# Performance work log

Measured on AMD Instinct MI355X. Metric: run time of the kernel, lower is better.

The kernel has to match this reference:

```python
import jax, jax.numpy as jnp
import numpy as np

N_EMBD = 768
N_HEAD = 12
HEAD_DIM = N_EMBD // N_HEAD  # 64


def apply_rotary_emb(x, cos, sin):
    d = x.shape[-1] // 2
    x1, x2 = x[..., :d], x[..., d:]
    y1 = x1 * cos + x2 * sin
    y2 = x1 * -sin + x2 * cos
    return jnp.concatenate([y1, y2], axis=-1)


def rms_norm(x):
    return x * jax.lax.rsqrt(jnp.mean(jnp.square(x), axis=-1, keepdims=True) + 1e-06)


def setup_inputs() -> dict:
    key = jax.random.key(0)
    ks = jax.random.split(key, 7)
    B, T = 2, 2048
    x = jax.random.normal(ks[0], (B, T, N_EMBD), dtype=jnp.float32)
    # cos/sin broadcast over (B, head) axes of [B, T, H, HEAD_DIM//2]
    cos = jax.random.uniform(ks[1], (T, 1, HEAD_DIM // 2), dtype=jnp.float32)
    sin = jax.random.uniform(ks[2], (T, 1, HEAD_DIM // 2), dtype=jnp.float32)
    scale = 1.0 / np.sqrt(N_EMBD)
    wq = jax.random.normal(ks[3], (N_EMBD, N_EMBD), dtype=jnp.float32) * scale
    wk = jax.random.normal(ks[4], (N_EMBD, N_EMBD), dtype=jnp.float32) * scale
    wv = jax.random.normal(ks[5], (N_EMBD, N_EMBD), dtype=jnp.float32) * scale
    wproj = jax.random.normal(ks[6], (N_EMBD, N_EMBD), dtype=jnp.float32) * scale
    return {"x": x, "cos": cos, "sin": sin, "wq": wq, "wk": wk, "wv": wv, "wproj": wproj}


def reference(x, cos, sin, wq, wk, wv, wproj):
    B, T, C = x.shape
    q = (x @ wq).reshape(B, T, N_HEAD, HEAD_DIM)
    k = (x @ wk).reshape(B, T, N_HEAD, HEAD_DIM)
    v = (x @ wv).reshape(B, T, N_HEAD, HEAD_DIM)
    q = rms_norm(apply_rotary_emb(q, cos, sin))
    k = rms_norm(apply_rotary_emb(k, cos, sin))
    # [B, H, T, T] attention scores (non-causal, as in source)
    attn = jnp.einsum('bqhd,bkhd->bhqk', q, k) / jnp.sqrt(jnp.float32(HEAD_DIM))
    attn = jax.nn.softmax(attn, axis=-1)
    y = jnp.einsum('bhqk,bkhd->bqhd', attn, v).reshape(B, T, C)
    return y @ wproj
```

## Files before the change

kernel.cpp:

```cpp
#include <hip/hip_runtime.h>
#include <hip/hip_bf16.h>
#include <stdint.h>

typedef __attribute__((ext_vector_type(8))) __bf16 bf16x8;
typedef __attribute__((ext_vector_type(4))) __bf16 bf16x4;
typedef __attribute__((ext_vector_type(2))) __bf16 bf16x2;
typedef __attribute__((ext_vector_type(4))) float f32x4;
typedef __attribute__((ext_vector_type(16))) float f32x16;
typedef __attribute__((ext_vector_type(8))) unsigned short u16x8;
typedef __attribute__((ext_vector_type(4))) unsigned int u32x4;

#define DEVI __device__ __forceinline__

DEVI void gload16(const void* g, void* l) {
  __builtin_amdgcn_global_load_lds((const __attribute__((address_space(1))) void*)g,
                                   (__attribute__((address_space(3))) void*)l, 16, 0, 0);
}

DEVI uint32_t pack2(float a, float b) {
  bf16x2 t;
  t[0] = (__bf16)a;
  t[1] = (__bf16)b;
  return __builtin_bit_cast(uint32_t, t);
}

DEVI int vswz(int d) { return ((d ^ (d >> 3)) & 15) << 4; }

__global__ __launch_bounds__(256) void prep_k(const float* __restrict__ x,
                                              const float* __restrict__ wq,
                                              const float* __restrict__ wk,
                                              const float* __restrict__ wv,
                                              const float* __restrict__ wp,
                                              __bf16* __restrict__ xb,
                                              __bf16* __restrict__ WT) {
  __shared__ float tile[32][33];
  const int bid = blockIdx.x, tid = threadIdx.x;
  if (bid < 2304) {
    const int z = bid / 576, r = bid % 576;
    const int bx = r % 24, by = r / 24;
    const float* W = (z == 0) ? wq : (z == 1) ? wk : (z == 2) ? wv : wp;
    int n0 = bx * 32, k0 = by * 32;
    int tx = tid & 31, ty = tid >> 5;
#pragma unroll
    for (int j = 0; j < 4; ++j)
      tile[ty + 8 * j][tx] = W[(size_t)(k0 + ty + 8 * j) * 768 + n0 + tx];
    __syncthreads();
#pragma unroll
    for (int j = 0; j < 4; ++j)
      WT[(size_t)(z * 768 + n0 + ty + 8 * j) * 768 + k0 + tx] =
          (__bf16)tile[tx][ty + 8 * j];
  } else {
    const int n4 = (4096 * 768) / 4;
    int i = (bid - 2304) * 256 + tid;
    for (; i < n4; i += 768 * 256) {
      float4 v = ((const float4*)x)[i];
      bf16x4 o;
      o[0] = (__bf16)v.x; o[1] = (__bf16)v.y; o[2] = (__bf16)v.z; o[3] = (__bf16)v.w;
      ((bf16x4*)xb)[i] = o;
    }
  }
}

template <int EPI, int BN>
__global__ __launch_bounds__(256) void gemm_k(const __bf16* __restrict__ A,
                                              const __bf16* __restrict__ B,
                                              void* __restrict__ Cout,
                                              const float* __restrict__ cosT,
                                              const float* __restrict__ sinT,
                                              int K, int lda, int ldb, int ldc,
                                              int nwg, int nxb) {
  constexpr int NF = BN / 32;
  constexpr int LPT = 2 + BN / 64;
  __shared__ __align__(16) __bf16 Al[4][128 * 32];
  __shared__ __align__(16) __bf16 Bl[4][BN * 32];
  const int tid = threadIdx.x, lane = tid & 63, w = tid >> 6;
  const int wm = w >> 1, wn = w & 1;
  const int bid = blockIdx.x;
  const int o = (bid & 7) * (nwg >> 3) + (bid >> 3);
  const int bx = o % nxb, by = o / nxb;
  const int m0 = by * 128, n0 = bx * BN;
  const int c = lane & 15, g = lane >> 4;
  f32x4 acc[4][NF] = {};

  auto stage = [&](int k0, int buf) {
#pragma unroll
    for (int i = 0; i < 2; ++i) {
      int e = (i * 256 + tid) * 8;
      int row = e >> 5, col = e & 31;
      gload16(A + (size_t)(m0 + row) * lda + k0 + col, (char*)&Al[buf][0] + 2 * (size_t)e);
    }
#pragma unroll
    for (int i = 0; i < BN / 64; ++i) {
      int e = (i * 256 + tid) * 8;
      int row = e >> 5, col = e & 31;
      gload16(B + (size_t)(n0 + row) * ldb + k0 + col, (char*)&Bl[buf][0] + 2 * (size_t)e);
    }
  };

  const int NIT = K / 32;
  stage(0, 0);
  stage(32, 1);
  for (int t = 0; t < NIT; ++t) {
    if (t + 2 < NIT) {
      stage((t + 2) * 32, (t + 2) & 3);
      asm volatile("s_waitcnt vmcnt(%0)" ::"i"(2 * LPT) : "memory");
    } else if (t + 1 < NIT) {
      asm volatile("s_waitcnt vmcnt(%0)" ::"i"(LPT) : "memory");
    } else {
      asm volatile("s_waitcnt vmcnt(0)" ::: "memory");
    }
    __builtin_amdgcn_s_barrier();
    const int cur = t & 3;
    bf16x8 af[4], bfr[NF];
#pragma unroll
    for (int q = 0; q < 4; ++q)
      af[q] = *(const bf16x8*)&Al[cur][(wm * 64 + q * 16 + c) * 32 + 8 * g];
#pragma unroll
    for (int q = 0; q < NF; ++q)
      bfr[q] = *(const bf16x8*)&Bl[cur][(wn * (BN / 2) + q * 16 + c) * 32 + 8 * g];
#pragma unroll
    for (int mf = 0; mf < 4; ++mf)
#pragma unroll
      for (int nf = 0; nf < NF; ++nf)
        acc[mf][nf] = __builtin_amdgcn_mfma_f32_16x16x32_bf16(af[mf], bfr[nf],
                                                              acc[mf][nf], 0, 0, 0);
  }

  if (EPI == 1) {
    __bf16* out = (__bf16*)Cout;
    const int colbase = n0 + wn * 64;
    const int plane = colbase / 768;
#pragma unroll
    for (int mf = 0; mf < 4; ++mf) {
#pragma unroll
      for (int r = 0; r < 4; ++r) {
        int row = m0 + wm * 64 + mf * 16 + 4 * g + r;
        float v0 = acc[mf][0][r], v1 = acc[mf][1][r], v2 = acc[mf][2][r], v3 = acc[mf][3][r];
        float y0, y1, y2, y3;
        if (plane < 2) {
          int t = row & 2047;
          float c0 = cosT[t * 32 + c],      s0 = sinT[t * 32 + c];
          float c1 = cosT[t * 32 + 16 + c], s1 = sinT[t * 32 + 16 + c];
          y0 = v0 * c0 + v2 * s0;
          y2 = v2 * c0 - v0 * s0;
          y1 = v1 * c1 + v3 * s1;
          y3 = v3 * c1 - v1 * s1;
          float ss = y0 * y0 + y1 * y1 + y2 * y2 + y3 * y3;
          ss += __shfl_xor(ss, 1); ss += __shfl_xor(ss, 2);
          ss += __shfl_xor(ss, 4); ss += __shfl_xor(ss, 8);
          float rn = rsqrtf(ss * (1.0f / 64.0f) + 1e-6f);
          y0 *= rn; y1 *= rn; y2 *= rn; y3 *= rn;
        } else {
          y0 = v0; y1 = v1; y2 = v2; y3 = v3;
        }
        size_t base = (size_t)row * ldc + colbase + c;
        out[base +  0] = (__bf16)y0;
        out[base + 16] = (__bf16)y1;
        out[base + 32] = (__bf16)y2;
        out[base + 48] = (__bf16)y3;
      }
    }
  } else {
    float* out = (float*)Cout;
#pragma unroll
    for (int mf = 0; mf < 4; ++mf)
#pragma unroll
      for (int nf = 0; nf < NF; ++nf)
#pragma unroll
        for (int r = 0; r < 4; ++r) {
          int row = m0 + wm * 64 + mf * 16 + 4 * g + r;
          out[(size_t)row * ldc + n0 + wn * (BN / 2) + nf * 16 + c] = acc[mf][nf][r];
        }
  }
}

__global__ __launch_bounds__(256, 2) void attn_k(const __bf16* __restrict__ QKV,
                                                 __bf16* __restrict__ Yb) {
  constexpr int TT = 2048, KVB = 128, NT = TT / KVB;
  __shared__ __align__(16) char smem[65536];
  const int tid = threadIdx.x, lane = tid & 63, w = tid >> 6;
  const int q5 = lane & 31, h = lane >> 5;
  const int bid = blockIdx.x;
  const int xcd = bid & 7, idx = bid >> 3;
  const int bh = xcd * 3 + (idx >> 4), qb = idx & 15;
  const int b = bh / 12, hd = bh % 12;
  const size_t ldq = 2304;
  const __bf16* Qg = QKV + (size_t)(b * TT) * ldq + hd * 64;
  const __bf16* Kg = QKV + (size_t)(b * TT) * ldq + 768 + hd * 64;
  const __bf16* Vg = QKV + (size_t)(b * TT) * ldq + 1536 + hd * 64;

  const int qrow = qb * 128 + w * 32 + q5;
  bf16x8 aq[4];
#pragma unroll
  for (int t = 0; t < 4; ++t)
    aq[t] = *(const bf16x8*)(Qg + (size_t)qrow * ldq + t * 16 + 8 * h);

  u16x8 vr[4];
  auto stageK = [&](int kv0, int buf) {
#pragma unroll
    for (int p = 0; p < 4; ++p) {
      int cid = p * 256 + tid;
      int row = cid >> 3, s = cid & 7;
      int srccol = 8 * (s ^ (row & 7));
      gload16(Kg + (size_t)(kv0 + row) * ldq + srccol,
              smem + buf * 16384 + row * 128 + 16 * s);
    }
  };
  auto loadV = [&](int kv0) {
#pragma unroll
    for (int p = 0; p < 2; ++p) {
      int u = p * 256 + tid;
      int kp = u >> 3, d0 = (u & 7) * 8;
      const __bf16* src0 = Vg + (size_t)(kv0 + 2 * kp) * ldq + d0;
      vr[2 * p] = *(const u16x8*)src0;
      vr[2 * p + 1] = *(const u16x8*)(src0 + ldq);
    }
  };
  auto writeV = [&](int buf) {
    char* vb = smem + 32768 + buf * 16384;
#pragma unroll
    for (int p = 0; p < 2; ++p) {
      int u = p * 256 + tid;
      int kp = u >> 3, d0 = (u & 7) * 8;
#pragma unroll
      for (int i = 0; i < 8; ++i) {
        int d = d0 + i;
        int byte = (d * 256 + 4 * kp) ^ vswz(d);
        uint32_t pk = (uint32_t)vr[2 * p][i] | ((uint32_t)vr[2 * p + 1][i] << 16);
        *(uint32_t*)(vb + byte) = pk;
      }
    }
  };

  f32x16 Yacc[2] = {};
  const float SC = 0.18033688f;
  float m2 = -__builtin_inff(), l_run = 0.f;

  stageK(0, 0);
  loadV(0);
  writeV(0);
  __syncthreads();

  f32x16 Sv[4];
#define SV(i) Sv[(i) >> 4][(i) & 15]

  for (int t = 0; t < NT; ++t) {
    const int cur = t & 1;
    const char* Kb = smem + cur * 16384;
    const char* Vb = smem + 32768 + cur * 16384;
    if (t + 1 < NT) {
      stageK((t + 1) * KVB, cur ^ 1);
      loadV((t + 1) * KVB);
    }

#pragma unroll
    for (int j = 0; j < 4; ++j) {
      f32x16 S = {};
#pragma unroll
      for (int tt = 0; tt < 4; ++tt) {
        int row = j * 32 + q5;
        int chunk = (2 * tt + h) ^ (q5 & 7);
        bf16x8 kf = *(const bf16x8*)(Kb + row * 128 + 16 * chunk);
        S = __builtin_amdgcn_mfma_f32_32x32x16_bf16(kf, aq[tt], S, 0, 0, 0);
      }
      Sv[j] = S;
    }

    float m0 = SV(0), m1 = SV(1), m2c = SV(2), m3 = SV(3);
#pragma unroll
    for (int i = 4; i < 64; i += 4) {
      m0 = fmaxf(m0, SV(i));       m1 = fmaxf(m1, SV(i + 1));
      m2c = fmaxf(m2c, SV(i + 2)); m3 = fmaxf(m3, SV(i + 3));
    }
    float mx = fmaxf(fmaxf(m0, m1), fmaxf(m2c, m3));
    mx = fmaxf(mx, __shfl_xor(mx, 32));
    mx *= SC;
    if (!__all(mx <= m2 + 8.0f)) {
      float mn = fmaxf(m2, mx);
      float corr = __builtin_exp2f(m2 - mn);
      l_run *= corr;
#pragma unroll
      for (int dh = 0; dh < 2; ++dh)
#pragma unroll
        for (int r = 0; r < 16; ++r) Yacc[dh][r] *= corr;
      m2 = mn;
    }
    float rs0 = 0.f, rs1 = 0.f, rs2 = 0.f, rs3 = 0.f;
#pragma unroll
    for (int i = 0; i < 64; i += 4) {
      float e0 = __builtin_exp2f(fmaf(SV(i), SC, -m2));
      float e1 = __builtin_exp2f(fmaf(SV(i + 1), SC, -m2));
      float e2 = __builtin_exp2f(fmaf(SV(i + 2), SC, -m2));
      float e3 = __builtin_exp2f(fmaf(SV(i + 3), SC, -m2));
      SV(i) = e0; SV(i + 1) = e1; SV(i + 2) = e2; SV(i + 3) = e3;
      rs0 += e0; rs1 += e1; rs2 += e2; rs3 += e3;
    }
    float rs = (rs0 + rs1) + (rs2 + rs3);
    rs += __shfl_xor(rs, 32);
    l_run += rs;

#pragma unroll
    for (int j = 0; j < 4; ++j) {
#pragma unroll
      for (int s = 0; s < 2; ++s) {
        int e0 = j * 16 + s * 8;
        uint32_t pk01 = pack2(SV(e0 + 0), SV(e0 + 1));
        uint32_t pk23 = pack2(SV(e0 + 2), SV(e0 + 3));
        uint32_t pk45 = pack2(SV(e0 + 4), SV(e0 + 5));
        uint32_t pk67 = pack2(SV(e0 + 6), SV(e0 + 7));
        uint32_t fa = (uint32_t)__shfl_xor((int)(h ? pk01 : pk45), 32);
        uint32_t fb = (uint32_t)__shfl_xor((int)(h ? pk23 : pk67), 32);
        u32x4 pw;
        pw[0] = h ? fa : pk01;
        pw[1] = h ? fb : pk23;
        pw[2] = h ? pk45 : fa;
        pw[3] = h ? pk67 : fb;
        bf16x8 pfrag = __builtin_bit_cast(bf16x8, pw);
        int keyb = j * 64 + s * 32 + 16 * h;
#pragma unroll
        for (int dh = 0; dh < 2; ++dh) {
          int d = dh * 32 + q5;
          int byte = (d * 256 + keyb) ^ vswz(d);
          bf16x8 vf = *(const bf16x8*)(Vb + byte);
          Yacc[dh] = __builtin_amdgcn_mfma_f32_32x32x16_bf16(vf, pfrag, Yacc[dh], 0, 0, 0);
        }
      }
    }
    if (t + 1 < NT) writeV(cur ^ 1);
    __syncthreads();
  }
#undef SV

  float rl = __builtin_amdgcn_rcpf(l_run);
  char* yb = smem + w * (32 * 144);
#pragma unroll
  for (int dh = 0; dh < 2; ++dh)
#pragma unroll
    for (int a = 0; a < 4; ++a) {
      bf16x4 pkv;
#pragma unroll
      for (int i = 0; i < 4; ++i) pkv[i] = (__bf16)(Yacc[dh][a * 4 + i] * rl);
      int d0 = a * 8 + 4 * h + 32 * dh;
      *(bf16x4*)(yb + q5 * 144 + d0 * 2) = pkv;
    }
  __bf16* Yrow = Yb + (size_t)(b * TT + qb * 128 + w * 32) * 768 + hd * 64;
#pragma unroll
  for (int k = 0; k < 4; ++k) {
    int chunk = k * 64 + lane;
    int qr = chunk >> 3, sr = chunk & 7;
    bf16x8 vv = *(const bf16x8*)(yb + qr * 144 + sr * 16);
    *(bf16x8*)(Yrow + (size_t)qr * 768 + sr * 8) = vv;
  }
}

extern "C" void kernel_launch(void* const* d_in, const int* in_sizes, int n_in,
                              void* d_out, int out_size, void* d_ws, size_t ws_size,
                              hipStream_t stream) {
  const float* x = (const float*)d_in[0];
  const float* cosT = (const float*)d_in[1];
  const float* sinT = (const float*)d_in[2];
  const float* wq = (const float*)d_in[3];
  const float* wk = (const float*)d_in[4];
  const float* wv = (const float*)d_in[5];
  const float* wp = (const float*)d_in[6];

  char* ws = (char*)d_ws;
  __bf16* xb   = (__bf16*)(ws);
  __bf16* WT   = (__bf16*)(ws + 6291456);
  __bf16* QKVb = (__bf16*)(ws + 11010048);
  __bf16* Yb   = (__bf16*)(ws + 29884416);

  prep_k<<<3072, 256, 0, stream>>>(x, wq, wk, wv, wp, xb, WT);
  gemm_k<1, 128><<<576, 256, 0, stream>>>(xb, WT, (void*)QKVb, cosT, sinT,
                                          768, 768, 768, 2304, 576, 18);
  attn_k<<<384, 256, 0, stream>>>(QKVb, Yb);
  gemm_k<0, 64><<<384, 256, 0, stream>>>(Yb, WT + (size_t)2304 * 768, d_out,
                                         nullptr, nullptr, 768, 768, 768, 768, 384, 12);
}
```

Baseline: 200.7 us.

## Write V transposed from QKV GEMM epilogue and stage it via async LDS loads

New measurement: 190.7 us. 5.0% less time.

```diff
diff --git a/kernel.cpp b/kernel.cpp
--- a/kernel.cpp
+++ b/kernel.cpp
@@ -7,7 +7,6 @@
 typedef __attribute__((ext_vector_type(2))) __bf16 bf16x2;
 typedef __attribute__((ext_vector_type(4))) float f32x4;
 typedef __attribute__((ext_vector_type(16))) float f32x16;
-typedef __attribute__((ext_vector_type(8))) unsigned short u16x8;
 typedef __attribute__((ext_vector_type(4))) unsigned int u32x4;
 
 #define DEVI __device__ __forceinline__
@@ -23,8 +22,6 @@
   t[1] = (__bf16)b;
   return __builtin_bit_cast(uint32_t, t);
 }
-
-DEVI int vswz(int d) { return ((d ^ (d >> 3)) & 15) << 4; }
 
 __global__ __launch_bounds__(256) void prep_k(const float* __restrict__ x,
                                               const float* __restrict__ wq,
@@ -65,6 +62,7 @@
 __global__ __launch_bounds__(256) void gemm_k(const __bf16* __restrict__ A,
                                               const __bf16* __restrict__ B,
                                               void* __restrict__ Cout,
+                                              __bf16* __restrict__ Vt,
                                               const float* __restrict__ cosT,
                                               const float* __restrict__ sinT,
                                               int K, int lda, int ldb, int ldc,
@@ -127,37 +125,48 @@
   }
 
   if (EPI == 1) {
-    __bf16* out = (__bf16*)Cout;
     const int colbase = n0 + wn * 64;
     const int plane = colbase / 768;
-#pragma unroll
-    for (int mf = 0; mf < 4; ++mf) {
-#pragma unroll
-      for (int r = 0; r < 4; ++r) {
-        int row = m0 + wm * 64 + mf * 16 + 4 * g + r;
-        float v0 = acc[mf][0][r], v1 = acc[mf][1][r], v2 = acc[mf][2][r], v3 = acc[mf][3][r];
-        float y0, y1, y2, y3;
-        if (plane < 2) {
+    if (plane == 2) {
+      const int hd = (colbase - 1536) >> 6;
+#pragma unroll
+      for (int mf = 0; mf < 4; ++mf)
+#pragma unroll
+        for (int nf = 0; nf < 4; ++nf) {
+          bf16x4 pk;
+#pragma unroll
+          for (int r = 0; r < 4; ++r) pk[r] = (__bf16)acc[mf][nf][r];
+          int row = m0 + wm * 64 + mf * 16 + 4 * g;
+          int bb = row >> 11, tloc = row & 2047;
+          int d = nf * 16 + c;
+          *(bf16x4*)(Vt + ((size_t)(bb * 12 + hd) * 64 + d) * 2048 + tloc) = pk;
+        }
+    } else {
+      __bf16* out = (__bf16*)Cout;
+#pragma unroll
+      for (int mf = 0; mf < 4; ++mf) {
+#pragma unroll
+        for (int r = 0; r < 4; ++r) {
+          int row = m0 + wm * 64 + mf * 16 + 4 * g + r;
+          float v0 = acc[mf][0][r], v1 = acc[mf][1][r], v2 = acc[mf][2][r], v3 = acc[mf][3][r];
           int t = row & 2047;
           float c0 = cosT[t * 32 + c],      s0 = sinT[t * 32 + c];
           float c1 = cosT[t * 32 + 16 + c], s1 = sinT[t * 32 + 16 + c];
-          y0 = v0 * c0 + v2 * s0;
-          y2 = v2 * c0 - v0 * s0;
-          y1 = v1 * c1 + v3 * s1;
-          y3 = v3 * c1 - v1 * s1;
+          float y0 = v0 * c0 + v2 * s0;
+          float y2 = v2 * c0 - v0 * s0;
+          float y1 = v1 * c1 + v3 * s1;
+          float y3 = v3 * c1 - v1 * s1;
           float ss = y0 * y0 + y1 * y1 + y2 * y2 + y3 * y3;
           ss += __shfl_xor(ss, 1); ss += __shfl_xor(ss, 2);
           ss += __shfl_xor(ss, 4); ss += __shfl_xor(ss, 8);
           float rn = rsqrtf(ss * (1.0f / 64.0f) + 1e-6f);
           y0 *= rn; y1 *= rn; y2 *= rn; y3 *= rn;
-        } else {
-          y0 = v0; y1 = v1; y2 = v2; y3 = v3;
+          size_t base = (size_t)row * ldc + colbase + c;
+          out[base +  0] = (__bf16)y0;
+          out[base + 16] = (__bf16)y1;
+          out[base + 32] = (__bf16)y2;
+          out[base + 48] = (__bf16)y3;
         }
-        size_t base = (size_t)row * ldc + colbase + c;
-        out[base +  0] = (__bf16)y0;
-        out[base + 16] = (__bf16)y1;
-        out[base + 32] = (__bf16)y2;
-        out[base + 48] = (__bf16)y3;
       }
     }
   } else {
@@ -174,20 +183,19 @@
   }
 }
 
-__global__ __launch_bounds__(256, 2) void attn_k(const __bf16* __restrict__ QKV,
+__global__ __launch_bounds__(256, 2) void attn_k(const __bf16* __restrict__ QK,
+                                                 const __bf16* __restrict__ Vt,
                                                  __bf16* __restrict__ Yb) {
   constexpr int TT = 2048, KVB = 128, NT = TT / KVB;
   __shared__ __align__(16) char smem[65536];
   const int tid = threadIdx.x, lane = tid & 63, w = tid >> 6;
   const int q5 = lane & 31, h = lane >> 5;
-  const int bid = blockIdx.x;
-  const int xcd = bid & 7, idx = bid >> 3;
-  const int bh = xcd * 3 + (idx >> 4), qb = idx & 15;
+  const int qb = blockIdx.x, bh = blockIdx.y;
   const int b = bh / 12, hd = bh % 12;
-  const size_t ldq = 2304;
-  const __bf16* Qg = QKV + (size_t)(b * TT) * ldq + hd * 64;
-  const __bf16* Kg = QKV + (size_t)(b * TT) * ldq + 768 + hd * 64;
-  const __bf16* Vg = QKV + (size_t)(b * TT) * ldq + 1536 + hd * 64;
+  const size_t ldq = 1536;
+  const __bf16* Qg = QK + (size_t)(b * TT) * ldq + hd * 64;
+  const __bf16* Kg = QK + (size_t)(b * TT) * ldq + 768 + hd * 64;
+  const __bf16* Vtg = Vt + (size_t)(b * 12 + hd) * 64 * 2048;
 
   const int qrow = qb * 128 + w * 32 + q5;
   bf16x8 aq[4];
@@ -195,40 +203,22 @@
   for (int t = 0; t < 4; ++t)
     aq[t] = *(const bf16x8*)(Qg + (size_t)qrow * ldq + t * 16 + 8 * h);
 
-  u16x8 vr[4];
   auto stageK = [&](int kv0, int buf) {
 #pragma unroll
     for (int p = 0; p < 4; ++p) {
       int cid = p * 256 + tid;
       int row = cid >> 3, s = cid & 7;
-      int srccol = 8 * (s ^ (row & 7));
-      gload16(Kg + (size_t)(kv0 + row) * ldq + srccol,
-              smem + buf * 16384 + row * 128 + 16 * s);
+      gload16(Kg + (size_t)(kv0 + row) * ldq + 8 * (s ^ (row & 7)),
+              smem + buf * 16384 + cid * 16);
     }
   };
-  auto loadV = [&](int kv0) {
-#pragma unroll
-    for (int p = 0; p < 2; ++p) {
-      int u = p * 256 + tid;
-      int kp = u >> 3, d0 = (u & 7) * 8;
-      const __bf16* src0 = Vg + (size_t)(kv0 + 2 * kp) * ldq + d0;
-      vr[2 * p] = *(const u16x8*)src0;
-      vr[2 * p + 1] = *(const u16x8*)(src0 + ldq);
-    }
-  };
-  auto writeV = [&](int buf) {
-    char* vb = smem + 32768 + buf * 16384;
-#pragma unroll
-    for (int p = 0; p < 2; ++p) {
-      int u = p * 256 + tid;
-      int kp = u >> 3, d0 = (u & 7) * 8;
-#pragma unroll
-      for (int i = 0; i < 8; ++i) {
-        int d = d0 + i;
-        int byte = (d * 256 + 4 * kp) ^ vswz(d);
-        uint32_t pk = (uint32_t)vr[2 * p][i] | ((uint32_t)vr[2 * p + 1][i] << 16);
-        *(uint32_t*)(vb + byte) = pk;
-      }
+  auto stageVt = [&](int kv0, int buf) {
+#pragma unroll
+    for (int p = 0; p < 4; ++p) {
+      int cid = p * 256 + tid;
+      int row = cid >> 4, cc = cid & 15;
+      gload16(Vtg + (size_t)row * 2048 + kv0 + 8 * (cc ^ (row & 15)),
+              smem + 32768 + buf * 16384 + cid * 16);
     }
   };
 
@@ -237,8 +227,7 @@
   float m2 = -__builtin_inff(), l_run = 0.f;
 
   stageK(0, 0);
-  loadV(0);
-  writeV(0);
+  stageVt(0, 0);
   __syncthreads();
 
   f32x16 Sv[4];
@@ -250,7 +239,7 @@
     const char* Vb = smem + 32768 + cur * 16384;
     if (t + 1 < NT) {
       stageK((t + 1) * KVB, cur ^ 1);
-      loadV((t + 1) * KVB);
+      stageVt((t + 1) * KVB, cur ^ 1);
     }
 
 #pragma unroll
@@ -316,17 +305,15 @@
         pw[2] = h ? pk45 : fa;
         pw[3] = h ? pk67 : fb;
         bf16x8 pfrag = __builtin_bit_cast(bf16x8, pw);
-        int keyb = j * 64 + s * 32 + 16 * h;
+        int lc = j * 4 + s * 2 + h;
 #pragma unroll
         for (int dh = 0; dh < 2; ++dh) {
-          int d = dh * 32 + q5;
-          int byte = (d * 256 + keyb) ^ vswz(d);
+          int byte = (dh * 32 + q5) * 256 + 16 * (lc ^ (q5 & 15));
           bf16x8 vf = *(const bf16x8*)(Vb + byte);
           Yacc[dh] = __builtin_amdgcn_mfma_f32_32x32x16_bf16(vf, pfrag, Yacc[dh], 0, 0, 0);
         }
       }
     }
-    if (t + 1 < NT) writeV(cur ^ 1);
     __syncthreads();
   }
 #undef SV
@@ -365,15 +352,16 @@
   const float* wp = (const float*)d_in[6];
 
   char* ws = (char*)d_ws;
-  __bf16* xb   = (__bf16*)(ws);
-  __bf16* WT   = (__bf16*)(ws + 6291456);
-  __bf16* QKVb = (__bf16*)(ws + 11010048);
-  __bf16* Yb   = (__bf16*)(ws + 29884416);
+  __bf16* xb  = (__bf16*)(ws);
+  __bf16* WT  = (__bf16*)(ws + 6291456);
+  __bf16* QKb = (__bf16*)(ws + 11010048);
+  __bf16* Vt  = (__bf16*)(ws + 23592960);
+  __bf16* Yb  = (__bf16*)(ws + 29884416);
 
   prep_k<<<3072, 256, 0, stream>>>(x, wq, wk, wv, wp, xb, WT);
-  gemm_k<1, 128><<<576, 256, 0, stream>>>(xb, WT, (void*)QKVb, cosT, sinT,
-                                          768, 768, 768, 2304, 576, 18);
-  attn_k<<<384, 256, 0, stream>>>(QKVb, Yb);
-  gemm_k<0, 64><<<384, 256, 0, stream>>>(Yb, WT + (size_t)2304 * 768, d_out,
+  gemm_k<1, 128><<<576, 256, 0, stream>>>(xb, WT, (void*)QKb, Vt, cosT, sinT,
+                                          768, 768, 768, 1536, 576, 18);
+  attn_k<<<dim3(16, 24), 256, 0, stream>>>(QKb, Vt, Yb);
+  gemm_k<0, 64><<<384, 256, 0, stream>>>(Yb, WT + (size_t)2304 * 768, d_out, nullptr,
                                          nullptr, nullptr, 768, 768, 768, 768, 384, 12);
 }
```
